# Optimization experiments

Hardware: AMD Instinct MI355X
Metric: run time of the kernel (lower is better)

## Reference

```python
import jax, jax.numpy as jnp
import numpy as np
import math

HID = 300   # model dim (d_k in the source's scale factor)
HDIM = 64   # attention projection dim
NH = 8      # heads = last axis of view(B,S,HDIM//8,8)
DH = HDIM // NH
L = 6


def pos_encoding(S, d):
    pos = jnp.arange(S, dtype=jnp.float32)[:, None]
    i = jnp.arange(d)
    expo = jnp.where(i % 2 == 0, i, i - 1).astype(jnp.float32) / d
    ang = pos / jnp.power(jnp.float32(10000.0), expo)  # (S, d)
    return jnp.where(i % 2 == 0, jnp.sin(ang), jnp.cos(ang))


def norm(x, g, b):
    mu = jnp.mean(x, axis=-1, keepdims=True)
    var = jnp.var(x, axis=-1, keepdims=True, ddof=1)  # torch.var is unbiased
    return g * (x - mu) / jnp.sqrt(var + 1e-8) + b


def mha(x, mask, wq, wk, wv, wo):
    B, S, _ = x.shape
    # view(B,S,DH,NH).permute(3,0,1,2): head h = feature indices i*NH+h
    q = (x @ wq).reshape(B, S, DH, NH).transpose(3, 0, 1, 2)  # (NH,B,S,DH)
    k = (x @ wk).reshape(B, S, DH, NH).transpose(3, 0, 1, 2)
    v = (x @ wv).reshape(B, S, DH, NH).transpose(3, 0, 1, 2)
    e = jnp.einsum('hbqd,hbkd->hbqk', q, k) / math.sqrt(HID)
    e = jnp.where(mask[None], jnp.float32(-1e9), e)
    alpha = jax.nn.softmax(e, axis=-1)
    h = jnp.einsum('hbqk,hbkd->hbqd', alpha, v)
    # cat(head0..head7, dim=2) -> head-major feature layout
    a = h.transpose(1, 2, 0, 3).reshape(B, S, HDIM)
    return a @ wo


def encoder(x, mask, wq, wk, wv, wo, w1, bb1, w2, bb2, g1, be1, g2, be2):
    x2 = mha(x, mask, wq, wk, wv, wo)
    x = norm(x2 + x, g1, be1)
    ff = jnp.maximum(x @ w1 + bb1, 0.0) @ w2 + bb2
    x = norm(ff + x, g2, be2)
    return x


def setup_inputs() -> dict:
    key = jax.random.key(0)
    ks = jax.random.split(key, 16)
    B, S, V, C = 32, 512, 50000, 1000
    sc = 0.02
    return {
        'x': jax.random.randint(ks[0], (B, S), 0, V),
        'emb': jax.random.normal(ks[1], (V, HID), jnp.float32) * sc,
        'WQ': jax.random.normal(ks[2], (L, HID, HDIM), jnp.float32) * sc,
        'WK': jax.random.normal(ks[3], (L, HID, HDIM), jnp.float32) * sc,
        'WV': jax.random.normal(ks[4], (L, HID, HDIM), jnp.float32) * sc,
        'WO': jax.random.normal(ks[5], (L, HDIM, HID), jnp.float32) * sc,
        'W1': jax.random.normal(ks[6], (L, HID, 4 * HID), jnp.float32) * sc,
        'b1': jax.random.normal(ks[7], (L, 4 * HID), jnp.float32) * sc,
        'W2': jax.random.normal(ks[8], (L, 4 * HID, HID), jnp.float32) * sc,
        'b2': jax.random.normal(ks[9], (L, HID), jnp.float32) * sc,
        'gamma1': jnp.ones((L,), jnp.float32),
        'beta1': jnp.zeros((L,), jnp.float32),
        'gamma2': jnp.ones((L,), jnp.float32),
        'beta2': jnp.zeros((L,), jnp.float32),
        'V_d': jax.random.normal(ks[10], (HID, C), jnp.float32) * sc,
        'gamma_f': jnp.float32(1.0),
        'beta_f': jnp.float32(0.0),
    }


def reference(x, emb, WQ, WK, WV, WO, W1, b1, W2, b2,
              gamma1, beta1, gamma2, beta2, V_d, gamma_f, beta_f):
    B, S = x.shape
    mask = (x == 0)[:, None, :] * jnp.ones((1, S, 1), bool)  # (B,S,S)
    x1 = emb[x]                               # (B,S,HID)
    x2 = x1 + pos_encoding(S, HID)[None]
    acc = x2 + x1                             # dense residual running sum
    out = x2
    for l in range(L):
        out = encoder(acc, mask, WQ[l], WK[l], WV[l], WO[l],
                      W1[l], b1[l], W2[l], b2[l],
                      gamma1[l], beta1[l], gamma2[l], beta2[l])
        acc = acc + out
    logits = jnp.sum(out, axis=1) @ V_d       # (B,C)
    return jax.nn.softmax(norm(logits, gamma_f, beta_f), axis=1)
```

## Files before the change

kernel.cpp:

```cpp
#include <hip/hip_runtime.h>
#include <hip/hip_bf16.h>
#include <cstdio>
#include <cstdint>

#define BATCH 32
#define SEQ 512
#define BSQ (BATCH*SEQ)
#define HIDD 300
#define HD 64
#define NHEAD 8
#define DHEAD 8
#define NLAYERS 6
#define FFD 1200
#define NCLS 1000
#define NSPLIT 4
#define KCH (SEQ/NSPLIT)
#define CLS_KS 4
#define CLS_KC (HIDD/CLS_KS)

typedef short short8 __attribute__((ext_vector_type(8)));
typedef float floatx4 __attribute__((ext_vector_type(4)));

__device__ __forceinline__ short f2b(float v){
  __hip_bfloat16 h = __float2bfloat16(v);
  short s; __builtin_memcpy(&s, &h, 2); return s;
}
__device__ __forceinline__ unsigned pk2(float a, float b){
  return (unsigned)(unsigned short)f2b(a) | ((unsigned)(unsigned short)f2b(b) << 16);
}

__global__ void t10_embed(const int* __restrict__ toks,
                          const float* __restrict__ emb,
                          float* __restrict__ acc,
                          short* __restrict__ accbf){
  int idx = blockIdx.x*256 + threadIdx.x;
  if (idx >= BSQ*320) return;
  int row = idx / 320;
  int j   = idx - row*320;
  if (j >= HIDD){ accbf[(size_t)row*320 + j] = 0; return; }
  int t = toks[row];
  float e = emb[(size_t)t*HIDD + j];
  int s = row & (SEQ-1);
  float expo = (float)(j & ~1) * (1.0f/(float)HIDD);
  float ang  = (float)s * expf(-expo * 9.210340371976184f);
  float pe   = (j & 1) ? cosf(ang) : sinf(ang);
  float v = 2.0f*e + pe;
  acc[(size_t)row*HIDD + j] = v;
  accbf[(size_t)row*320 + j] = f2b(v);
}

__global__ void prep_w(const float* __restrict__ src, short* __restrict__ dst,
                       int K, int N, int Kpad, int rows, int nbase,
                       int sls, int dls, int total, int perm){
  int idx = blockIdx.x*256 + threadIdx.x;
  if (idx >= total) return;
  int l   = idx / (rows*Kpad);
  int rem = idx - l*(rows*Kpad);
  int n = rem / Kpad;
  int k = rem - n*Kpad;
  int sc = perm ? ((n & 7)*8 + (n >> 3)) : n;
  float v = (n < N && k < K) ? src[(size_t)l*sls + (size_t)k*N + sc] : 0.f;
  dst[(size_t)l*dls + (size_t)(nbase+n)*Kpad + k] = f2b(v);
}

__global__ __launch_bounds__(256) void mm_a16(
    const short* __restrict__ A, const short* __restrict__ Wt,
    const float* __restrict__ bias, float* __restrict__ C,
    short* __restrict__ Cb,
    int M, int N, int Kpad, int Npad, int nnb, int relu){
  __shared__ short sA[64][40];
  __shared__ short sB[64][40];
  int wg = blockIdx.x;
  int cpx = gridDim.x >> 3;
  int swz = (wg & 7)*cpx + (wg >> 3);
  int mt = swz / nnb, nt = swz - mt*nnb;
  int m0 = mt*64, n0 = nt*64;
  int tid = threadIdx.x;
  int lane = tid & 63, wv = tid >> 6;
  int wm = (wv & 1)*32, wn = (wv >> 1)*32;
  int l15 = lane & 15, quad = lane >> 4;
  floatx4 acc[2][2] = {};
  int srow = tid >> 2, sko = (tid & 3)*8;
  const short* Arow = A  + (size_t)(m0 + srow)*Kpad + sko;
  const short* Brow = Wt + (size_t)(n0 + srow)*Kpad + sko;
  int nch = Kpad >> 5;
  for (int c = 0; c < nch; c++){
    int k0 = c*32;
    __syncthreads();
    *(short8*)&sA[srow][sko] = *(const short8*)(Arow + k0);
    *(short8*)&sB[srow][sko] = *(const short8*)(Brow + k0);
    __syncthreads();
    short8 af[2], bf[2];
    for (int i=0;i<2;i++)
      af[i] = *(const short8*)&sA[wm + i*16 + l15][quad*8];
    for (int j=0;j<2;j++)
      bf[j] = *(const short8*)&sB[wn + j*16 + l15][quad*8];
    for (int i=0;i<2;i++)
      for (int j=0;j<2;j++)
        acc[i][j] = __builtin_amdgcn_mfma_f32_16x16x32_bf16(af[i], bf[j], acc[i][j], 0,0,0);
  }
  if (Cb){
    for (int j=0;j<2;j++){
      int n = n0 + wn + j*16 + l15;
      float bv = (bias && n < N) ? bias[n] : 0.f;
      for (int i=0;i<2;i++){
        int mbase = m0 + wm + i*16 + quad*4;
        for (int r=0;r<4;r++){
          float cv = acc[i][j][r] + bv;
          if (relu) cv = fmaxf(cv, 0.f);
          Cb[(size_t)(mbase+r)*Npad + n] = (n < N) ? f2b(cv) : (short)0;
        }
      }
    }
  } else {
    for (int j=0;j<2;j++){
      int n = n0 + wn + j*16 + l15;
      if (n >= N) continue;
      float bv = bias ? bias[n] : 0.f;
      for (int i=0;i<2;i++){
        int mbase = m0 + wm + i*16 + quad*4;
        for (int r=0;r<4;r++){
          float cv = acc[i][j][r] + bv;
          if (relu) cv = fmaxf(cv, 0.f);
          C[(size_t)(mbase+r)*N + n] = cv;
        }
      }
    }
  }
}

__global__ __launch_bounds__(256) void t14_attn(
    const float* __restrict__ qkv, const int* __restrict__ toks,
    float* __restrict__ pp, float* __restrict__ ps){
  __shared__ float kb[KCH][9];
  __shared__ float vb[KCH][9];
  __shared__ float msk[KCH];
  __shared__ short Pl[4][16][136];
  int blk = blockIdx.x;
  int ks = blk & (NSPLIT-1);
  int bh = blk >> 2;
  int b = bh >> 3, h = bh & 7;
  int tid = threadIdx.x;
  int lane = tid & 63, w = tid >> 6;
  int quad = lane >> 4, l15 = lane & 15;
  int kbase = ks*KCH;
  {
    int r = tid >> 1, half = (tid & 1)*4;
    const float* src = qkv + (size_t)(b*SEQ + kbase + r)*192 + h*8 + half;
    float4 kx = *(const float4*)(src + 64);
    float4 vx = *(const float4*)(src + 128);
    kb[r][half+0]=kx.x; kb[r][half+1]=kx.y; kb[r][half+2]=kx.z; kb[r][half+3]=kx.w;
    vb[r][half+0]=vx.x; vb[r][half+1]=vx.y; vb[r][half+2]=vx.z; vb[r][half+3]=vx.w;
  }
  if (tid < KCH)
    msk[tid] = (toks[b*SEQ + kbase + tid]==0) ? -1e9f : 0.f;
  __syncthreads();

  short8 kfrag[8];
  #pragma unroll
  for (int kt=0;kt<8;kt++){
    short8 f; 
    #pragma unroll
    for (int j=0;j<8;j++) f[j] = 0;
    if (quad == 0){
      #pragma unroll
      for (int j=0;j<8;j++) f[j] = f2b(kb[kt*16 + l15][j]);
    }
    kfrag[kt] = f;
  }
  short8 vfrag[4];
  #pragma unroll
  for (int ks2=0;ks2<4;ks2++){
    short8 f;
    #pragma unroll
    for (int j=0;j<8;j++) f[j] = 0;
    if (l15 < 8){
      #pragma unroll
      for (int j=0;j<8;j++) f[j] = f2b(vb[ks2*32 + quad*8 + j][l15]);
    } else if (l15 == 8){
      #pragma unroll
      for (int j=0;j<8;j++) f[j] = (short)0x3F80;
    }
    vfrag[ks2] = f;
  }
  const float scale = 0.057735026918962574f;

  for (int t = 0; t < 8; t++){
    int q0 = w*128 + t*16;
    short8 qf;
    #pragma unroll
    for (int j=0;j<8;j++) qf[j] = 0;
    if (quad == 0){
      const float* qsrc = qkv + (size_t)(b*SEQ + q0 + l15)*192 + h*8;
      float4 a = *(const float4*)qsrc;
      float4 c = *(const float4*)(qsrc + 4);
      qf[0]=f2b(a.x*scale); qf[1]=f2b(a.y*scale); qf[2]=f2b(a.z*scale); qf[3]=f2b(a.w*scale);
      qf[4]=f2b(c.x*scale); qf[5]=f2b(c.y*scale); qf[6]=f2b(c.z*scale); qf[7]=f2b(c.w*scale);
    }
    #pragma unroll
    for (int kt2 = 0; kt2 < 4; kt2++){
      floatx4 z = {0.f,0.f,0.f,0.f};
      floatx4 a0 = __builtin_amdgcn_mfma_f32_16x16x32_bf16(kfrag[2*kt2],   qf, z, 0,0,0);
      floatx4 a1 = __builtin_amdgcn_mfma_f32_16x16x32_bf16(kfrag[2*kt2+1], qf, z, 0,0,0);
      float p0[4], p1[4];
      #pragma unroll
      for (int r=0;r<4;r++){
        float m0 = msk[(2*kt2)*16   + quad*4 + r];
        float m1 = msk[(2*kt2+1)*16 + quad*4 + r];
        p0[r] = __expf(fminf(a0[r] + m0, 60.f));
        p1[r] = __expf(fminf(a1[r] + m1, 60.f));
      }
      uint2 u0, u1;
      u0.x = pk2(p0[0], p0[1]); u0.y = pk2(p0[2], p0[3]);
      u1.x = pk2(p1[0], p1[1]); u1.y = pk2(p1[2], p1[3]);
      *(uint2*)&Pl[w][l15][(2*kt2)*16   + quad*4] = u0;
      *(uint2*)&Pl[w][l15][(2*kt2+1)*16 + quad*4] = u1;
    }
    floatx4 o = {0.f,0.f,0.f,0.f};
    #pragma unroll
    for (int ks2=0; ks2<4; ks2++){
      short8 pa = *(const short8*)&Pl[w][l15][ks2*32 + quad*8];
      o = __builtin_amdgcn_mfma_f32_16x16x32_bf16(pa, vfrag[ks2], o, 0,0,0);
    }
    if (l15 < 8){
      #pragma unroll
      for (int r=0;r<4;r++){
        int q = q0 + quad*4 + r;
        pp[(size_t)ks*BSQ*64 + (size_t)(b*SEQ+q)*64 + h*8 + l15] = o[r];
      }
    } else if (l15 == 8){
      #pragma unroll
      for (int r=0;r<4;r++){
        int q = q0 + quad*4 + r;
        ps[(size_t)ks*BSQ*8 + (size_t)(b*SEQ+q)*8 + h] = o[r];
      }
    }
  }
}

__global__ __launch_bounds__(256) void t12_attn_comb(
    const float* __restrict__ pp, const float* __restrict__ ps,
    short* __restrict__ aout){
  int idx = blockIdx.x*256 + threadIdx.x;
  if (idx >= BSQ*8) return;
  float s = 0.f;
  for (int k=0;k<NSPLIT;k++) s += ps[(size_t)k*BSQ*8 + idx];
  float inv = 1.f/s;
  int bsq = idx >> 3, h = idx & 7;
  size_t base = (size_t)bsq*64 + h*8;
  float o[8] = {};
  for (int k=0;k<NSPLIT;k++){
    const float4* p = (const float4*)(pp + (size_t)k*BSQ*64 + base);
    float4 a = p[0], bq = p[1];
    o[0]+=a.x; o[1]+=a.y; o[2]+=a.z; o[3]+=a.w;
    o[4]+=bq.x; o[5]+=bq.y; o[6]+=bq.z; o[7]+=bq.w;
  }
  short8 r;
  for (int d=0;d<8;d++) r[d] = f2b(o[d]*inv);
  *(short8*)(aout + base) = r;
}

__global__ __launch_bounds__(256) void t10_addnorm(
                 const float* __restrict__ xa, const float* __restrict__ xb,
                 float* __restrict__ y, short* __restrict__ ybf,
                 float* __restrict__ accum, short* __restrict__ accbf,
                 const float* __restrict__ gamma, const float* __restrict__ beta,
                 int l){
  __shared__ float red[8];
  int row = blockIdx.x, tid = threadIdx.x;
  size_t base = (size_t)row*HIDD;
  size_t bbase = (size_t)row*320;
  float v0 = xa[base+tid] + xb[base+tid];
  float v1 = 0.f;
  int has1 = (tid+256 < HIDD);
  if (has1) v1 = xa[base+tid+256] + xb[base+tid+256];
  float s = v0+v1, sq = v0*v0+v1*v1;
  for (int off=32; off; off>>=1){ s += __shfl_down(s,off); sq += __shfl_down(sq,off); }
  int lane = tid & 63, w = tid >> 6;
  if (lane==0){ red[w]=s; red[4+w]=sq; }
  __syncthreads();
  float sum = red[0]+red[1]+red[2]+red[3];
  float ssq = red[4]+red[5]+red[6]+red[7];
  float mu  = sum * (1.0f/HIDD);
  float var = (ssq - (float)HIDD*mu*mu) * (1.0f/(HIDD-1));
  float rstd = rsqrtf(var + 1e-8f);
  float g = gamma[l], be = beta[l];
  float o0 = g*(v0-mu)*rstd + be;
  y[base+tid] = o0;
  if (ybf) ybf[bbase+tid] = f2b(o0);
  if (accum){
    float a0 = accum[base+tid] + o0;
    accum[base+tid] = a0;
    if (accbf) accbf[bbase+tid] = f2b(a0);
  }
  if (has1){
    float o1 = g*(v1-mu)*rstd + be;
    y[base+tid+256] = o1;
    if (ybf) ybf[bbase+tid+256] = f2b(o1);
    if (accum){
      float a1 = accum[base+tid+256] + o1;
      accum[base+tid+256] = a1;
      if (accbf) accbf[bbase+tid+256] = f2b(a1);
    }
  } else if (tid+256 < 320){
    if (ybf) ybf[bbase+tid+256] = 0;
    if (accbf) accbf[bbase+tid+256] = 0;
  }
}

__global__ __launch_bounds__(256) void t13_colsum_part(
    const float* __restrict__ outb, float* __restrict__ part){
  int blk = blockIdx.x;
  int b = blk >> 3, c = blk & 7;
  int tid = threadIdx.x;
  size_t base = (size_t)b*SEQ*HIDD + (size_t)c*64*HIDD;
  int j1 = tid + 256;
  float s0 = 0.f, s1 = 0.f;
  for (int t = 0; t < 64; t++){
    const float* row = outb + base + (size_t)t*HIDD;
    s0 += row[tid];
    if (j1 < HIDD) s1 += row[j1];
  }
  float* dst = part + (size_t)(c*BATCH + b)*HIDD;
  dst[tid] = s0;
  if (j1 < HIDD) dst[j1] = s1;
}

__global__ void t13_colsum_comb(const float* __restrict__ part,
                                float* __restrict__ sums){
  int idx = blockIdx.x*256 + threadIdx.x;
  if (idx >= BATCH*HIDD) return;
  float s = 0.f;
  for (int c = 0; c < 8; c++) s += part[(size_t)c*BATCH*HIDD + idx];
  sums[idx] = s;
}

__global__ __launch_bounds__(256) void t13_cls(
    const float* __restrict__ sums, const float* __restrict__ W,
    float* __restrict__ plog){
  int gid = blockIdx.x*256 + threadIdx.x;
  if (gid >= CLS_KS*BATCH*NCLS) return;
  int c = gid / (BATCH*NCLS);
  int rem = gid - c*(BATCH*NCLS);
  int m = rem / NCLS, n = rem - m*NCLS;
  const float* arow = sums + m*HIDD + c*CLS_KC;
  const float* wcol = W + (size_t)c*CLS_KC*NCLS + n;
  float acc = 0.f;
  #pragma unroll 5
  for (int k = 0; k < CLS_KC; k++)
    acc = fmaf(arow[k], wcol[(size_t)k*NCLS], acc);
  plog[gid] = acc;
}

__device__ __forceinline__ float t10_bsum(float val, float* red){
  for (int off=32; off; off>>=1) val += __shfl_down(val, off);
  __syncthreads();
  if ((threadIdx.x & 63)==0) red[threadIdx.x>>6] = val;
  __syncthreads();
  return red[0]+red[1]+red[2]+red[3];
}
__device__ __forceinline__ float t10_bmax(float val, float* red){
  for (int off=32; off; off>>=1) val = fmaxf(val, __shfl_down(val, off));
  __syncthreads();
  if ((threadIdx.x & 63)==0) red[threadIdx.x>>6] = val;
  __syncthreads();
  return fmaxf(fmaxf(red[0],red[1]), fmaxf(red[2],red[3]));
}

__global__ __launch_bounds__(256) void t10_final(
                  const float* __restrict__ plog,
                  const float* __restrict__ gf, const float* __restrict__ bff,
                  float* __restrict__ outp){
  __shared__ float red[4];
  int b = blockIdx.x, tid = threadIdx.x;
  size_t base = (size_t)b*NCLS;
  float v[4];
  float s = 0.f, sq = 0.f;
  for (int t=0;t<4;t++){
    int j = tid + t*256;
    float x = 0.f;
    if (j < NCLS){
      for (int c=0;c<CLS_KS;c++) x += plog[(size_t)c*BATCH*NCLS + base + j];
    }
    v[t] = x; s += x; sq += x*x;
  }
  s  = t10_bsum(s, red);
  sq = t10_bsum(sq, red);
  float mu  = s * (1.0f/NCLS);
  float var = (sq - (float)NCLS*mu*mu) * (1.0f/(NCLS-1));
  float rstd = rsqrtf(var + 1e-8f);
  float g = gf[0], be = bff[0];
  float y[4]; float mx = -1e30f;
  for (int t=0;t<4;t++){
    int j = tid + t*256;
    y[t] = g*(v[t]-mu)*rstd + be;
    if (j < NCLS) mx = fmaxf(mx, y[t]);
  }
  mx = t10_bmax(mx, red);
  float p[4]; float es = 0.f;
  for (int t=0;t<4;t++){
    int j = tid + t*256;
    p[t] = (j < NCLS) ? __expf(y[t]-mx) : 0.f;
    es += p[t];
  }
  es = t10_bsum(es, red);
  float inv = 1.0f/es;
  for (int t=0;t<4;t++){
    int j = tid + t*256;
    if (j < NCLS) outp[base+j] = p[t]*inv;
  }
}

extern "C" void kernel_launch(void* const* d_in, const int* in_sizes, int n_in,
                              void* d_out, int out_size, void* d_ws, size_t ws_size,
                              hipStream_t stream){
  const int*   toks = (const int*)d_in[0];
  const float* emb  = (const float*)d_in[1];
  const float* WQ   = (const float*)d_in[2];
  const float* WK   = (const float*)d_in[3];
  const float* WV   = (const float*)d_in[4];
  const float* WO   = (const float*)d_in[5];
  const float* W1   = (const float*)d_in[6];
  const float* b1   = (const float*)d_in[7];
  const float* W2   = (const float*)d_in[8];
  const float* b2   = (const float*)d_in[9];
  const float* g1   = (const float*)d_in[10];
  const float* be1  = (const float*)d_in[11];
  const float* g2   = (const float*)d_in[12];
  const float* be2  = (const float*)d_in[13];
  const float* Vd   = (const float*)d_in[14];
  const float* gf   = (const float*)d_in[15];
  const float* bff  = (const float*)d_in[16];
  float* outp = (float*)d_out;

  float* acc    = (float*)d_ws;
  float* xn     = acc    + (size_t)BSQ*HIDD;
  float* outb   = xn     + (size_t)BSQ*HIDD;
  float* tmp    = outb   + (size_t)BSQ*HIDD;
  float* qkv    = tmp    + (size_t)BSQ*HIDD;
  float* sums   = qkv    + (size_t)BSQ*192;
  float* logits = sums   + BATCH*HIDD;
  float* pp     = tmp;
  float* ps     = tmp + (size_t)NSPLIT*BSQ*64;
  short* acc_bf = (short*)(logits + BATCH*NCLS);
  short* xn_bf  = acc_bf + (size_t)BSQ*320;
  short* aat_bf = xn_bf  + (size_t)BSQ*320;
  short* ff1_bf = aat_bf + (size_t)BSQ*64;
  short* wqkv = ff1_bf + (size_t)BSQ*1216;
  short* wo   = wqkv + (size_t)6*192*320;
  short* w1t  = wo   + (size_t)6*320*64;
  short* w2t  = w1t  + (size_t)6*1216*320;
  float* cspart = (float*)(w2t + (size_t)6*320*1216);
  float* plog   = cspart + (size_t)8*BATCH*HIDD;

  {
    int tq = 6*64*320;
    prep_w<<<(tq+255)/256,256,0,stream>>>(WQ, wqkv, 300, 64, 320, 64, 0,   19200, 61440, tq, 1);
    prep_w<<<(tq+255)/256,256,0,stream>>>(WK, wqkv, 300, 64, 320, 64, 64,  19200, 61440, tq, 1);
    prep_w<<<(tq+255)/256,256,0,stream>>>(WV, wqkv, 300, 64, 320, 64, 128, 19200, 61440, tq, 1);
    int to = 6*320*64;
    prep_w<<<(to+255)/256,256,0,stream>>>(WO, wo, 64, 300, 64, 320, 0, 19200, 20480, to, 0);
    int t1 = 6*1216*320;
    prep_w<<<(t1+255)/256,256,0,stream>>>(W1, w1t, 300, 1200, 320, 1216, 0, 360000, 389120, t1, 0);
    int t2 = 6*320*1216;
    prep_w<<<(t2+255)/256,256,0,stream>>>(W2, w2t, 1200, 300, 1216, 320, 0, 360000, 389120, t2, 0);
  }

  t10_embed<<<(BSQ*320+255)/256, 256, 0, stream>>>(toks, emb, acc, acc_bf);

  for (int l = 0; l < NLAYERS; l++){
    mm_a16<<<256*3,256,0,stream>>>(acc_bf, wqkv + (size_t)l*61440, nullptr, qkv, nullptr,
                                   BSQ, 192, 320, 0, 3, 0);
    t14_attn<<<BATCH*NHEAD*NSPLIT, 256, 0, stream>>>(qkv, toks, pp, ps);
    t12_attn_comb<<<(BSQ*8)/256, 256, 0, stream>>>(pp, ps, aat_bf);
    mm_a16<<<256*5,256,0,stream>>>(aat_bf, wo + (size_t)l*20480, nullptr, tmp, nullptr,
                                   BSQ, 300, 64, 0, 5, 0);
    t10_addnorm<<<BSQ,256,0,stream>>>(tmp, acc, xn, xn_bf, nullptr, nullptr, g1, be1, l);
    mm_a16<<<256*19,256,0,stream>>>(xn_bf, w1t + (size_t)l*389120, b1 + (size_t)l*FFD,
                                    nullptr, ff1_bf, BSQ, 1200, 320, 1216, 19, 1);
    mm_a16<<<256*5,256,0,stream>>>(ff1_bf, w2t + (size_t)l*389120, b2 + (size_t)l*HIDD,
                                   tmp, nullptr, BSQ, 300, 1216, 0, 5, 0);
    t10_addnorm<<<BSQ,256,0,stream>>>(tmp, xn, outb, nullptr, acc, acc_bf, g2, be2, l);
  }

  t13_colsum_part<<<BATCH*8, 256, 0, stream>>>(outb, cspart);
  t13_colsum_comb<<<(BATCH*HIDD+255)/256, 256, 0, stream>>>(cspart, sums);
  t13_cls<<<(CLS_KS*BATCH*NCLS)/256, 256, 0, stream>>>(sums, Vd, plog);
  t10_final<<<BATCH, 256, 0, stream>>>(plog, gf, bff, outp);

  hipStreamCaptureStatus cs = hipStreamCaptureStatusNone;
  hipStreamIsCapturing(stream, &cs);
  if (cs == hipStreamCaptureStatusNone){
    hipError_t e_sync = hipStreamSynchronize(stream);
    float ho[4] = {-1,-1,-1,-1};
    hipMemcpy(ho, d_out, 16, hipMemcpyDeviceToHost);
    fprintf(stderr, "[t14] sync=%s out[0..3]=%g,%g,%g,%g\n",
            hipGetErrorString(e_sync), ho[0], ho[1], ho[2], ho[3]);
    fflush(stderr);
  }
}
```

Measured before the change: 1.127 ms.

## Use 128x128 GEMM tiles with direct global-to-LDS async loads

New measurement: 1.159 ms. 2.8% more time.

```diff
diff --git a/kernel.cpp b/kernel.cpp
--- a/kernel.cpp
+++ b/kernel.cpp
@@ -28,6 +28,10 @@
 __device__ __forceinline__ unsigned pk2(float a, float b){
   return (unsigned)(unsigned short)f2b(a) | ((unsigned)(unsigned short)f2b(b) << 16);
 }
+
+#define ASYNC16(g, l) __builtin_amdgcn_global_load_lds( \
+  (const __attribute__((address_space(1))) unsigned int*)(g), \
+  (__attribute__((address_space(3))) unsigned int*)(l), 16, 0, 0)
 
 __global__ void t10_embed(const int* __restrict__ toks,
                           const float* __restrict__ emb,
@@ -63,48 +67,59 @@
   dst[(size_t)l*dls + (size_t)(nbase+n)*Kpad + k] = f2b(v);
 }
 
-__global__ __launch_bounds__(256) void mm_a16(
+__global__ __launch_bounds__(256) void mm128(
     const short* __restrict__ A, const short* __restrict__ Wt,
     const float* __restrict__ bias, float* __restrict__ C,
     short* __restrict__ Cb,
     int M, int N, int Kpad, int Npad, int nnb, int relu){
-  __shared__ short sA[64][40];
-  __shared__ short sB[64][40];
+  __shared__ short sA[128][32];
+  __shared__ short sB[128][32];
   int wg = blockIdx.x;
   int cpx = gridDim.x >> 3;
   int swz = (wg & 7)*cpx + (wg >> 3);
   int mt = swz / nnb, nt = swz - mt*nnb;
-  int m0 = mt*64, n0 = nt*64;
+  int m0 = mt*128, n0 = nt*128;
   int tid = threadIdx.x;
   int lane = tid & 63, wv = tid >> 6;
-  int wm = (wv & 1)*32, wn = (wv >> 1)*32;
+  int wm = (wv & 1)*64, wn = (wv >> 1)*64;
   int l15 = lane & 15, quad = lane >> 4;
-  floatx4 acc[2][2] = {};
-  int srow = tid >> 2, sko = (tid & 3)*8;
-  const short* Arow = A  + (size_t)(m0 + srow)*Kpad + sko;
-  const short* Brow = Wt + (size_t)(n0 + srow)*Kpad + sko;
+  floatx4 acc[4][4] = {};
+  int lr = tid >> 2, lc = (tid & 3)*8;
+  const short* Ab = A  + (size_t)(m0 + lr)*Kpad + lc;
+  const short* Bb = Wt + (size_t)(n0 + lr)*Kpad + lc;
+  char* sAb = (char*)sA + wv*1024;
+  char* sBb = (char*)sB + wv*1024;
   int nch = Kpad >> 5;
   for (int c = 0; c < nch; c++){
     int k0 = c*32;
     __syncthreads();
-    *(short8*)&sA[srow][sko] = *(const short8*)(Arow + k0);
-    *(short8*)&sB[srow][sko] = *(const short8*)(Brow + k0);
+    ASYNC16(Ab + k0,                    sAb);
+    ASYNC16(Ab + (size_t)64*Kpad + k0,  sAb + 4096);
+    ASYNC16(Bb + k0,                    sBb);
+    ASYNC16(Bb + (size_t)64*Kpad + k0,  sBb + 4096);
     __syncthreads();
-    short8 af[2], bf[2];
-    for (int i=0;i<2;i++)
+    short8 af[4], bfr[4];
+    #pragma unroll
+    for (int i=0;i<4;i++)
       af[i] = *(const short8*)&sA[wm + i*16 + l15][quad*8];
-    for (int j=0;j<2;j++)
-      bf[j] = *(const short8*)&sB[wn + j*16 + l15][quad*8];
-    for (int i=0;i<2;i++)
-      for (int j=0;j<2;j++)
-        acc[i][j] = __builtin_amdgcn_mfma_f32_16x16x32_bf16(af[i], bf[j], acc[i][j], 0,0,0);
+    #pragma unroll
+    for (int j=0;j<4;j++)
+      bfr[j] = *(const short8*)&sB[wn + j*16 + l15][quad*8];
+    #pragma unroll
+    for (int i=0;i<4;i++)
+      #pragma unroll
+      for (int j=0;j<4;j++)
+        acc[i][j] = __builtin_amdgcn_mfma_f32_16x16x32_bf16(af[i], bfr[j], acc[i][j], 0,0,0);
   }
   if (Cb){
-    for (int j=0;j<2;j++){
+    #pragma unroll
+    for (int j=0;j<4;j++){
       int n = n0 + wn + j*16 + l15;
       float bv = (bias && n < N) ? bias[n] : 0.f;
-      for (int i=0;i<2;i++){
+      #pragma unroll
+      for (int i=0;i<4;i++){
         int mbase = m0 + wm + i*16 + quad*4;
+        #pragma unroll
         for (int r=0;r<4;r++){
           float cv = acc[i][j][r] + bv;
           if (relu) cv = fmaxf(cv, 0.f);
@@ -113,12 +128,15 @@
       }
     }
   } else {
-    for (int j=0;j<2;j++){
+    #pragma unroll
+    for (int j=0;j<4;j++){
       int n = n0 + wn + j*16 + l15;
       if (n >= N) continue;
       float bv = bias ? bias[n] : 0.f;
-      for (int i=0;i<2;i++){
+      #pragma unroll
+      for (int i=0;i<4;i++){
         int mbase = m0 + wm + i*16 + quad*4;
+        #pragma unroll
         for (int r=0;r<4;r++){
           float cv = acc[i][j][r] + bv;
           if (relu) cv = fmaxf(cv, 0.f);
@@ -159,7 +177,7 @@
   short8 kfrag[8];
   #pragma unroll
   for (int kt=0;kt<8;kt++){
-    short8 f; 
+    short8 f;
     #pragma unroll
     for (int j=0;j<8;j++) f[j] = 0;
     if (quad == 0){
@@ -446,40 +464,41 @@
   short* xn_bf  = acc_bf + (size_t)BSQ*320;
   short* aat_bf = xn_bf  + (size_t)BSQ*320;
   short* ff1_bf = aat_bf + (size_t)BSQ*64;
-  short* wqkv = ff1_bf + (size_t)BSQ*1216;
-  short* wo   = wqkv + (size_t)6*192*320;
-  short* w1t  = wo   + (size_t)6*320*64;
-  short* w2t  = w1t  + (size_t)6*1216*320;
-  float* cspart = (float*)(w2t + (size_t)6*320*1216);
+  short* wqkv = ff1_bf + (size_t)BSQ*1280;
+  short* wo   = wqkv + (size_t)6*256*320;
+  short* w1t  = wo   + (size_t)6*384*64;
+  short* w2t  = w1t  + (size_t)6*1280*320;
+  float* cspart = (float*)(w2t + (size_t)6*384*1280);
   float* plog   = cspart + (size_t)8*BATCH*HIDD;
 
   {
     int tq = 6*64*320;
-    prep_w<<<(tq+255)/256,256,0,stream>>>(WQ, wqkv, 300, 64, 320, 64, 0,   19200, 61440, tq, 1);
-    prep_w<<<(tq+255)/256,256,0,stream>>>(WK, wqkv, 300, 64, 320, 64, 64,  19200, 61440, tq, 1);
-    prep_w<<<(tq+255)/256,256,0,stream>>>(WV, wqkv, 300, 64, 320, 64, 128, 19200, 61440, tq, 1);
-    int to = 6*320*64;
-    prep_w<<<(to+255)/256,256,0,stream>>>(WO, wo, 64, 300, 64, 320, 0, 19200, 20480, to, 0);
-    int t1 = 6*1216*320;
-    prep_w<<<(t1+255)/256,256,0,stream>>>(W1, w1t, 300, 1200, 320, 1216, 0, 360000, 389120, t1, 0);
-    int t2 = 6*320*1216;
-    prep_w<<<(t2+255)/256,256,0,stream>>>(W2, w2t, 1200, 300, 1216, 320, 0, 360000, 389120, t2, 0);
+    prep_w<<<(tq+255)/256,256,0,stream>>>(WQ, wqkv, 300, 64, 320, 64, 0,   19200, 81920, tq, 1);
+    prep_w<<<(tq+255)/256,256,0,stream>>>(WK, wqkv, 300, 64, 320, 64, 64,  19200, 81920, tq, 1);
+    prep_w<<<(tq+255)/256,256,0,stream>>>(WV, wqkv, 300, 64, 320, 64, 128, 19200, 81920, tq, 1);
+    prep_w<<<(tq+255)/256,256,0,stream>>>(WQ, wqkv, 300, 0,  320, 64, 192, 19200, 81920, tq, 0);
+    int to = 6*384*64;
+    prep_w<<<(to+255)/256,256,0,stream>>>(WO, wo, 64, 300, 64, 384, 0, 19200, 24576, to, 0);
+    int t1 = 6*1280*320;
+    prep_w<<<(t1+255)/256,256,0,stream>>>(W1, w1t, 300, 1200, 320, 1280, 0, 360000, 409600, t1, 0);
+    int t2 = 6*384*1280;
+    prep_w<<<(t2+255)/256,256,0,stream>>>(W2, w2t, 1200, 300, 1280, 384, 0, 360000, 491520, t2, 0);
   }
 
   t10_embed<<<(BSQ*320+255)/256, 256, 0, stream>>>(toks, emb, acc, acc_bf);
 
   for (int l = 0; l < NLAYERS; l++){
-    mm_a16<<<256*3,256,0,stream>>>(acc_bf, wqkv + (size_t)l*61440, nullptr, qkv, nullptr,
-                                   BSQ, 192, 320, 0, 3, 0);
+    mm128<<<128*2,256,0,stream>>>(acc_bf, wqkv + (size_t)l*81920, nullptr, qkv, nullptr,
+                                  BSQ, 192, 320, 0, 2, 0);
     t14_attn<<<BATCH*NHEAD*NSPLIT, 256, 0, stream>>>(qkv, toks, pp, ps);
     t12_attn_comb<<<(BSQ*8)/256, 256, 0, stream>>>(pp, ps, aat_bf);
-    mm_a16<<<256*5,256,0,stream>>>(aat_bf, wo + (size_t)l*20480, nullptr, tmp, nullptr,
-                                   BSQ, 300, 64, 0, 5, 0);
+    mm128<<<128*3,256,0,stream>>>(aat_bf, wo + (size_t)l*24576, nullptr, tmp, nullptr,
+                                  BSQ, 300, 64, 0, 3, 0);
     t10_addnorm<<<BSQ,256,0,stream>>>(tmp, acc, xn, xn_bf, nullptr, nullptr, g1, be1, l);
-    mm_a16<<<256*19,256,0,stream>>>(xn_bf, w1t + (size_t)l*389120, b1 + (size_t)l*FFD,
-                                    nullptr, ff1_bf, BSQ, 1200, 320, 1216, 19, 1);
-    mm_a16<<<256*5,256,0,stream>>>(ff1_bf, w2t + (size_t)l*389120, b2 + (size_t)l*HIDD,
-                                   tmp, nullptr, BSQ, 300, 1216, 0, 5, 0);
+    mm128<<<128*10,256,0,stream>>>(xn_bf, w1t + (size_t)l*409600, b1 + (size_t)l*FFD,
+                                   nullptr, ff1_bf, BSQ, 1200, 320, 1280, 10, 1);
+    mm128<<<128*3,256,0,stream>>>(ff1_bf, w2t + (size_t)l*491520, b2 + (size_t)l*HIDD,
+                                  tmp, nullptr, BSQ, 300, 1280, 0, 3, 0);
     t10_addnorm<<<BSQ,256,0,stream>>>(tmp, xn, outb, nullptr, acc, acc_bf, g2, be2, l);
   }
 
@@ -494,7 +513,7 @@
     hipError_t e_sync = hipStreamSynchronize(stream);
     float ho[4] = {-1,-1,-1,-1};
     hipMemcpy(ho, d_out, 16, hipMemcpyDeviceToHost);
-    fprintf(stderr, "[t14] sync=%s out[0..3]=%g,%g,%g,%g\n",
+    fprintf(stderr, "[t15] sync=%s out[0..3]=%g,%g,%g,%g\n",
             hipGetErrorString(e_sync), ho[0], ho[1], ho[2], ho[3]);
     fflush(stderr);
   }
```
